# Optimization experiments

Measured on AMD Instinct MI355X. Metric: run time of the kernel, lower is better.

## Reference

```python
import jax, jax.numpy as jnp
import numpy as np

ORDER = 2
TEMP = 1.0
NEG = -9e15


def setup_inputs() -> dict:
    key = jax.random.key(0)
    ks = jax.random.split(key, 12)
    B, D, N, L = 8, 64, 1024, 12
    C_OUT, NH, S = 64, 2, 2
    NOUT = (NH + 1) * ORDER * S + 1  # 13
    sc = 0.05
    x = jax.random.normal(ks[0], (B, D, N, L), jnp.float32)
    A = jax.random.uniform(ks[1], (S, N, N), jnp.float32)
    support = jnp.where(A > 0.9, A, 0.0)
    nv1 = jax.random.normal(ks[2], (N, D), jnp.float32)
    nv2 = jax.random.normal(ks[3], (D, N), jnp.float32)
    key_w = jax.random.normal(ks[4], (NH, 2 * C_OUT, D, L), jnp.float32) * sc
    key_b = jax.random.normal(ks[5], (NH, 2 * C_OUT), jnp.float32) * sc
    query_w = jax.random.normal(ks[6], (NH, 2 * C_OUT, D, L), jnp.float32) * sc
    query_b = jax.random.normal(ks[7], (NH, 2 * C_OUT), jnp.float32) * sc
    attn_w = jax.random.normal(ks[8], (NOUT, D * NOUT), jnp.float32) * sc
    attn_b = jax.random.normal(ks[9], (NOUT,), jnp.float32) * sc
    final_w = jax.random.normal(ks[10], (C_OUT, D), jnp.float32) * sc
    final_b = jax.random.normal(ks[11], (C_OUT,), jnp.float32) * sc
    return {"x": x, "support": support, "nv1": nv1, "nv2": nv2,
            "key_w": key_w, "key_b": key_b, "query_w": query_w, "query_b": query_b,
            "attn_w": attn_w, "attn_b": attn_b, "final_w": final_w, "final_b": final_b}


def reference(x, support, nv1, nv2, key_w, key_b, query_w, query_b,
              attn_w, attn_b, final_w, final_b):
    B, D, N, L = x.shape
    n_head = key_w.shape[0]
    # spatial PE broadcast: nv1 [N,D] -> [1,D,N,1], nv2 [D,N] -> [1,D,N,1]
    nv1_b = nv1.T[None, :, :, None]
    nv2_b = nv2[None, :, :, None]
    out = [x]
    for s in range(support.shape[0]):
        a = support[s]  # [N,N]
        for ih in range(n_head + 1):
            if ih == 0:
                x1 = x
                for _ in range(ORDER):
                    # x2[b,d,w,l] = sum_v x1[b,d,v,l] * a[v,w]
                    x1 = jnp.einsum('bdvl,vw->bdwl', x1, a)
                    out.append(x1)
            else:
                ki = x + nv1_b
                qi = x + nv2_b
                # Conv2d(c_in, 2*c_out, (1,L)) -> [B, 2*c_out, N]
                keys = jnp.einsum('bdnl,edl->ben', ki, key_w[ih - 1]) + key_b[ih - 1][None, :, None]
                query = jnp.einsum('bdnl,edl->ben', qi, query_w[ih - 1]) + query_b[ih - 1][None, :, None]
                e = jax.nn.relu(jnp.einsum('ben,bem->bnm', keys, query))  # [B,N,N]
                att = jnp.where(a[None] > 0, e, NEG) / TEMP
                att = jax.nn.softmax(att, axis=1)  # normalize over source nodes v
                x1 = x
                for _ in range(ORDER):
                    x1 = jnp.einsum('bdvl,bvw->bdwl', x1, att)
                    out.append(x1)
    H = len(out)  # nout
    # per-branch gating attention (is_attention=True)
    feats = jnp.stack([o.mean(axis=(2, 3)) for o in out], axis=1)  # [B,H,D]
    logits = feats.reshape(B, H * D) @ attn_w.T + attn_b  # [B,H]
    gate = jax.nn.softmax(logits / TEMP, axis=1)
    # SUM head aggregation of gated branches
    h = out[0] * gate[:, 0, None, None, None]
    for i in range(1, H):
        h = h + out[i] * gate[:, i, None, None, None]
    # final 1x1 conv
    h = jnp.einsum('bdnl,od->bonl', h, final_w) + final_b[None, :, None, None]
    return h
```

## Files before the change

### kernel.cpp

```cpp
#include <hip/hip_runtime.h>
#include <hip/hip_bf16.h>

#define BB 8
#define DD 64
#define NNODE 1024
#define LLL 12
#define EE 128
#define NEGV -9.0e15f

typedef _Float16 f16;
typedef _Float16 f16x4 __attribute__((ext_vector_type(4)));
typedef _Float16 f16x8 __attribute__((ext_vector_type(8)));
typedef float f32x4 __attribute__((ext_vector_type(4)));


__device__ __forceinline__ void stage_tile(const char* g, int ld, char* lds, int t) {
    int wid = t >> 6, lane = t & 63;
#pragma unroll
    for (int it = 0; it < 4; it++) {
        int cbase = it * 256 + wid * 64;
        int c = cbase + lane;
        int row = c >> 3, p = c & 7;
        int gch = p ^ (row & 7);
        const char* src = g + (size_t)row * ld + gch * 16;
        char* dst = lds + (size_t)cbase * 16;
        __builtin_amdgcn_global_load_lds(
            (const __attribute__((address_space(1))) unsigned int*)src,
            (__attribute__((address_space(3))) unsigned int*)dst, 16, 0, 0);
    }
}

__device__ __forceinline__ void mma_tile(const char* As, const char* Bs, int t,
                                         f32x4 acc[4][4]) {
    int lane = t & 63, wid = t >> 6;
    int wr = (wid >> 1) * 64, wc = (wid & 1) * 64;
    int lrow = lane & 15, lk = lane >> 4;
#pragma unroll
    for (int kk = 0; kk < 2; kk++) {
        f16x8 af[4], bf[4];
#pragma unroll
        for (int m = 0; m < 4; m++) {
            int row = wr + m * 16 + lrow;
            int p = (kk * 4 + lk) ^ (row & 7);
            af[m] = *(const f16x8*)(As + row * 128 + p * 16);
        }
#pragma unroll
        for (int n = 0; n < 4; n++) {
            int row = wc + n * 16 + lrow;
            int p = (kk * 4 + lk) ^ (row & 7);
            bf[n] = *(const f16x8*)(Bs + row * 128 + p * 16);
        }
#pragma unroll
        for (int m = 0; m < 4; m++)
#pragma unroll
            for (int n = 0; n < 4; n++)
                acc[m][n] = __builtin_amdgcn_mfma_f32_16x16x32_f16(
                    af[m], bf[n], acc[m][n], 0, 0, 0);
    }
}

__device__ __forceinline__ void zero_acc(f32x4 acc[4][4]) {
#pragma unroll
    for (int m = 0; m < 4; m++)
#pragma unroll
        for (int n = 0; n < 4; n++)
#pragma unroll
            for (int q = 0; q < 4; q++) acc[m][n][q] = 0.f;
}

__device__ __forceinline__ const f16* pair_B(const f16* aT, const f16* attT,
                                             int j, int b) {
    if (j == 0) return aT;
    if (j == 3) return aT + 1048576;
    int idx = (j < 3) ? (j - 1) : (j - 2);
    return attT + (size_t)idx * 8388608 + (size_t)b * 1048576;
}


__global__ __launch_bounds__(256) void k_xtfused(const float* __restrict__ x,
                                                 f16* __restrict__ XT,
                                                 f16* __restrict__ xT2,
                                                 float* __restrict__ xl) {
    __shared__ f16 Ls[64][210];
    int nt = blockIdx.x, d0 = blockIdx.y * 16, b = blockIdx.z;
    int n0 = nt * 64, t = threadIdx.x;
    for (int f = t; f < 3072; f += 256) {
        int dd = f / 192, rem = f - dd * 192, j = rem / 3, q = rem - j * 3;
        float4 v = *reinterpret_cast<const float4*>(
            x + (((size_t)(b * 64 + d0 + dd) * 1024) + n0 + j) * 12 + q * 4);
        f16* dst = &Ls[j][dd * 12 + q * 4];
        dst[0] = (f16)v.x; dst[1] = (f16)v.y; dst[2] = (f16)v.z; dst[3] = (f16)v.w;
    }
    __syncthreads();
    for (int c = t; c < 12288; c += 256) {
        int row = c >> 6, j = c & 63;
        int dd = row / 12, l = row - dd * 12;
        XT[((size_t)(b * 768) + (size_t)(d0 + dd) * 12 + l) * 1024 + n0 + j] =
            Ls[j][row];
    }
    for (int c = t; c < 1536; c += 256) {
        int j = c / 24, p = c - j * 24;
        *reinterpret_cast<f16x8*>(
            xT2 + ((size_t)(b * 1024) + n0 + j) * 768 + d0 * 12 + p * 8) =
            *reinterpret_cast<const f16x8*>(&Ls[j][p * 8]);
    }
    for (int c = t; c < 1024; c += 256) {
        int dd = c >> 6, j = c & 63;
        float s = 0.f;
#pragma unroll
        for (int l = 0; l < 12; l++) s += (float)Ls[j][dd * 12 + l];
        xl[((size_t)(b * 64 + d0 + dd)) * 1024 + n0 + j] = s;
    }
}

__global__ void k_wcvt(const float* __restrict__ kw, const float* __restrict__ qw,
                       float* __restrict__ kwl, f16* __restrict__ kwb) {
    int i = blockIdx.x * 256 + threadIdx.x;
    int d = i & 63, e = (i >> 6) & 127, var = i >> 13;
    const float* src = (var < 2 ? kw + (size_t)var * 98304
                                : qw + (size_t)(var - 2) * 98304) +
                       ((size_t)e * 64 + d) * 12;
    f16* dst = kwb + ((size_t)var * 128 + e) * 768 + d * 12;
    float ssum = 0.f;
#pragma unroll
    for (int l = 0; l < 12; l++) {
        float v = src[l];
        ssum += v;
        dst[l] = (f16)v;
    }
    kwl[i] = ssum;
}

__global__ void k_tkq(const float* __restrict__ kwl, const float* __restrict__ nv1,
                      const float* __restrict__ nv2, const float* __restrict__ kb,
                      const float* __restrict__ qb, float* __restrict__ tkq) {
    int i = blockIdx.x * 256 + threadIdx.x;
    int e = i & 127, n = (i >> 7) & 1023, var = i >> 17;
    float ssum = (var < 2) ? kb[var * 128 + e] : qb[(var - 2) * 128 + e];
    const float* wl = kwl + ((size_t)var * 128 + e) * 64;
    if (var < 2) {
        const float* nvp = nv1 + (size_t)n * 64;
#pragma unroll 8
        for (int d = 0; d < 64; d++) ssum += wl[d] * nvp[d];
    } else {
#pragma unroll 8
        for (int d = 0; d < 64; d++) ssum += wl[d] * nv2[(size_t)d * 1024 + n];
    }
    tkq[i] = ssum;
}

__global__ void k_acvt(const float* __restrict__ sup, f16* __restrict__ aT) {
    __shared__ float Ls[64][65];
    int s = blockIdx.z, v0 = blockIdx.y * 64, w0 = blockIdx.x * 64, t = threadIdx.x;
    int j = t & 63, i0 = t >> 6;
    for (int i = i0; i < 64; i += 4)
        Ls[i][j] = sup[((size_t)s * 1024 + v0 + i) * 1024 + w0 + j];
    __syncthreads();
    for (int i = i0; i < 64; i += 4)
        aT[((size_t)s * 1024 + w0 + i) * 1024 + v0 + j] = (f16)Ls[j][i];
}


__global__ __launch_bounds__(256) void k_kqgemm(const f16* __restrict__ xT2,
                                                const f16* __restrict__ kwb,
                                                const float* __restrict__ tkq,
                                                f16* __restrict__ keysT) {
    __shared__ char As[16384], Bs[16384];
    int z = blockIdx.z, var = z >> 3, b = z & 7;
    int nt = blockIdx.x, t = threadIdx.x;
    const char* Ag = (const char*)(xT2 + ((size_t)b * 1024 + nt * 128) * 768);
    const char* Bg = (const char*)(kwb + (size_t)var * 128 * 768);
    f32x4 acc[4][4];
    zero_acc(acc);
    for (int kt = 0; kt < 12; kt++) {
        stage_tile(Ag + kt * 128, 1536, As, t);
        stage_tile(Bg + kt * 128, 1536, Bs, t);
        __syncthreads();
        mma_tile(As, Bs, t, acc);
        __syncthreads();
    }
    int lane = t & 63, wid = t >> 6;
    int wr = (wid >> 1) * 64, wc = (wid & 1) * 64;
    int cn = lane & 15, rq = (lane >> 4) * 4;
#pragma unroll
    for (int m = 0; m < 4; m++)
#pragma unroll
        for (int q = 0; q < 4; q++) {
            int n_g = nt * 128 + wr + m * 16 + rq + q;
#pragma unroll
            for (int nn = 0; nn < 4; nn++) {
                int e = wc + nn * 16 + cn;
                float v = acc[m][nn][q] + tkq[((size_t)var * 1024 + n_g) * 128 + e];
                keysT[(((size_t)var * 8 + b) * 1024 + n_g) * 128 + e] = (f16)v;
            }
        }
}

__global__ __launch_bounds__(256) void k_scoregemm2(const f16* __restrict__ keysT,
                                                    f16* __restrict__ scTall) {
    __shared__ char As[16384], Bs[16384];
    int z = blockIdx.z, h = z >> 3, b = z & 7;
    int wt = blockIdx.y, vt = blockIdx.x, t = threadIdx.x;
    const char* Ag = (const char*)(keysT + (((size_t)(2 + h) * 8 + b) * 1024 + wt * 128) * 128);
    const char* Bg = (const char*)(keysT + (((size_t)h * 8 + b) * 1024 + vt * 128) * 128);
    f32x4 acc[4][4];
    zero_acc(acc);
    for (int kt = 0; kt < 2; kt++) {
        stage_tile(Ag + kt * 128, 256, As, t);
        stage_tile(Bg + kt * 128, 256, Bs, t);
        __syncthreads();
        mma_tile(As, Bs, t, acc);
        __syncthreads();
    }
    int lane = t & 63, wid = t >> 6;
    int wr = (wid >> 1) * 64, wc = (wid & 1) * 64;
    int cn = lane & 15, rq = (lane >> 4) * 4;
#pragma unroll
    for (int m = 0; m < 4; m++)
#pragma unroll
        for (int q = 0; q < 4; q++) {
            int w = wt * 128 + wr + m * 16 + rq + q;
#pragma unroll
            for (int nn = 0; nn < 4; nn++) {
                int v = vt * 128 + wc + nn * 16 + cn;
                scTall[((size_t)z * 1024 + w) * 1024 + v] = (f16)fmaxf(acc[m][nn][q], 0.f);
            }
        }
}

__global__ __launch_bounds__(256) void k_prop1m(const f16* __restrict__ ZT,
                                                const f16* __restrict__ aT,
                                                const f16* __restrict__ attT,
                                                f16* __restrict__ P1all) {
    __shared__ char As[16384], Bs[16384];
    int bid = blockIdx.x;
    int swz = (bid & 7) * 288 + (bid >> 3);
    int wt = swz & 7, rt = (swz >> 3) % 6, z = swz / 48;
    int j = z >> 3, b = z & 7;
    int t = threadIdx.x;
    const char* Ag = (const char*)(ZT + ((size_t)b * 768 + rt * 128) * 1024);
    const char* Bg = (const char*)(pair_B(aT, attT, j, b) + (size_t)wt * 128 * 1024);
    f32x4 acc[4][4];
    zero_acc(acc);
    for (int kt = 0; kt < 16; kt++) {
        stage_tile(Ag + kt * 128, 2048, As, t);
        stage_tile(Bg + kt * 128, 2048, Bs, t);
        __syncthreads();
        mma_tile(As, Bs, t, acc);
        __syncthreads();
    }
    f16* P1 = P1all + (size_t)j * 6291456;
    int lane = t & 63, wid = t >> 6;
    int wr = (wid >> 1) * 64, wc = (wid & 1) * 64;
    int cn = lane & 15, rq = (lane >> 4) * 4;
#pragma unroll
    for (int m = 0; m < 4; m++)
#pragma unroll
        for (int q = 0; q < 4; q++) {
            int r = rt * 128 + wr + m * 16 + rq + q;
            size_t pbase = ((size_t)b * 768 + r) * 1024;
#pragma unroll
            for (int nn = 0; nn < 4; nn++) {
                int w = wt * 128 + wc + nn * 16 + cn;
                P1[pbase + w] = (f16)acc[m][nn][q];
            }
        }
}

__global__ __launch_bounds__(256) void k_prop2m(const f16* __restrict__ P1all,
                                                const f16* __restrict__ aT,
                                                const f16* __restrict__ attT,
                                                f16* __restrict__ P2all) {
    __shared__ char As[16384], Bs[16384];
    int bid = blockIdx.x;
    int swz = (bid & 7) * 288 + (bid >> 3);
    int wt = swz & 7, rt = (swz >> 3) % 6, z = swz / 48;
    int j = z >> 3, b = z & 7;
    int t = threadIdx.x;
    const char* Ag = (const char*)(P1all + (size_t)j * 6291456 +
                                   ((size_t)b * 768 + rt * 128) * 1024);
    const char* Bg = (const char*)(pair_B(aT, attT, j, b) + (size_t)wt * 128 * 1024);
    f32x4 acc[4][4];
    zero_acc(acc);
    for (int kt = 0; kt < 16; kt++) {
        stage_tile(Ag + kt * 128, 2048, As, t);
        stage_tile(Bg + kt * 128, 2048, Bs, t);
        __syncthreads();
        mma_tile(As, Bs, t, acc);
        __syncthreads();
    }
    f16* P2 = P2all + (size_t)j * 6291456;
    int lane = t & 63, wid = t >> 6;
    int wr = (wid >> 1) * 64, wc = (wid & 1) * 64;
    int cn = lane & 15, rq = (lane >> 4) * 4;
#pragma unroll
    for (int m = 0; m < 4; m++)
#pragma unroll
        for (int q = 0; q < 4; q++) {
            int r = rt * 128 + wr + m * 16 + rq + q;
            size_t pbase = ((size_t)b * 768 + r) * 1024;
#pragma unroll
            for (int nn = 0; nn < 4; nn++) {
                int w = wt * 128 + wc + nn * 16 + cn;
                P2[pbase + w] = (f16)acc[m][nn][q];
            }
        }
}


__global__ void k_softmax3(const f16* __restrict__ scTall, const f16* __restrict__ aT,
                           f16* __restrict__ attT) {
    int gw = blockIdx.x * 4 + (threadIdx.x >> 6);
    int w = gw & 1023, hb = gw >> 10;
    int h = hb >> 3, b = hb & 7;
    int lane = threadIdx.x & 63;
    const f16* sp = scTall + (size_t)gw * 1024;
    float e[16];
#pragma unroll
    for (int k = 0; k < 16; k++) e[k] = (float)sp[k * 64 + lane];
#pragma unroll
    for (int s = 0; s < 2; s++) {
        const f16* ap = aT + ((size_t)s * 1024 + w) * 1024;
        float xx[16];
        float m = NEGV;
#pragma unroll
        for (int k = 0; k < 16; k++) {
            int v = k * 64 + lane;
            xx[k] = ((float)ap[v] > 0.f) ? e[k] : NEGV;
            m = fmaxf(m, xx[k]);
        }
#pragma unroll
        for (int off = 1; off < 64; off <<= 1) m = fmaxf(m, __shfl_xor(m, off));
        float ssum = 0.f;
#pragma unroll
        for (int k = 0; k < 16; k++) {
            xx[k] = __expf(xx[k] - m);
            ssum += xx[k];
        }
#pragma unroll
        for (int off = 1; off < 64; off <<= 1) ssum += __shfl_xor(ssum, off);
        float inv = 1.f / ssum;
        f16* op = attT + (size_t)(s * 2 + h) * 8388608 +
                  ((size_t)b * 1024 + w) * 1024;
#pragma unroll
        for (int k = 0; k < 16; k++) op[k * 64 + lane] = (f16)(xx[k] * inv);
    }
}

template <int ORDER>
__global__ __launch_bounds__(256) void k_colsum1(
    const f16* __restrict__ aT, const f16* __restrict__ attT,
    const float* __restrict__ ra, const float* __restrict__ ratt,
    float* __restrict__ partial) {
    int u = blockIdx.y, rc = blockIdx.x;
    int t = threadIdx.x;
    int lane7 = t & 127, rh = t >> 7;
    int v0 = lane7 * 8;
    const f16* M = (u < 2) ? aT + (size_t)u * 1048576
                           : attT + (size_t)(u - 2) * 1048576;
    const float* rin = nullptr;
    if (ORDER) rin = (u < 2) ? ra + (size_t)u * 2048 : ratt + (size_t)(u - 2) * 2048;
    float acc[8] = {};
    int row0 = rc * 64 + rh * 32;
#pragma unroll 4
    for (int i = 0; i < 32; i++) {
        int row = row0 + i;
        f16x8 mv = *reinterpret_cast<const f16x8*>(M + (size_t)row * 1024 + v0);
        float sc = ORDER ? rin[row] : 1.f;
#pragma unroll
        for (int j = 0; j < 8; j++) acc[j] += (float)mv[j] * sc;
    }
    float* pp = partial + ((size_t)u * 32 + rc * 2 + rh) * 1024 + v0;
#pragma unroll
    for (int j = 0; j < 8; j++) pp[j] = acc[j];
}

template <int ORDER>
__global__ void k_colsum2(const float* __restrict__ partial, float* __restrict__ ra,
                          float* __restrict__ ratt) {
    int u = blockIdx.x, t = threadIdx.x;
    for (int v = t; v < 1024; v += 256) {
        float s = 0.f;
#pragma unroll
        for (int k = 0; k < 32; k++) s += partial[((size_t)u * 32 + k) * 1024 + v];
        float* out = (u < 2) ? ra + (size_t)u * 2048 : ratt + (size_t)(u - 2) * 2048;
        out[ORDER * 1024 + v] = s;
    }
}

__global__ void k_feat13(const float* __restrict__ xl, const float* __restrict__ ra,
                         const float* __restrict__ ratt, float* __restrict__ feats) {
    int bd = blockIdx.x;
    int b = bd >> 6, d = bd & 63;
    const float* xp = xl + (size_t)bd * 1024;
    int t = threadIdx.x;
    float s[13];
#pragma unroll
    for (int i = 0; i < 13; i++) s[i] = 0.f;
    for (int v = t; v < 1024; v += 256) {
        float xv = xp[v];
        s[0] += xv;
#pragma unroll
        for (int ss = 0; ss < 2; ss++) {
            s[1 + ss * 6 + 0] += xv * ra[ss * 2048 + v];
            s[1 + ss * 6 + 1] += xv * ra[ss * 2048 + 1024 + v];
#pragma unroll
            for (int hh = 0; hh < 2; hh++) {
                const float* rb = ratt + (((size_t)(ss * 2 + hh) * 8 + b)) * 2048;
                s[1 + ss * 6 + 2 + hh * 2] += xv * rb[v];
                s[1 + ss * 6 + 3 + hh * 2] += xv * rb[1024 + v];
            }
        }
    }
    int wid = t >> 6, lane = t & 63;
#pragma unroll
    for (int i = 0; i < 13; i++)
#pragma unroll
        for (int off = 1; off < 64; off <<= 1) s[i] += __shfl_xor(s[i], off);
    __shared__ float red[13][4];
    if (lane == 0)
#pragma unroll
        for (int i = 0; i < 13; i++) red[i][wid] = s[i];
    __syncthreads();
    if (t < 13) {
        float tot = red[t][0] + red[t][1] + red[t][2] + red[t][3];
        feats[(size_t)b * 832 + t * 64 + d] = tot * (1.f / (1024.f * 12.f));
    }
}

__global__ void k_gate(const float* __restrict__ feats, const float* __restrict__ aw,
                       const float* __restrict__ ab, float* __restrict__ gate) {
    int b = blockIdx.x, t = threadIdx.x;
    __shared__ float lg[13];
    if (t < 13) {
        float s = ab[t];
        const float* f = feats + (size_t)b * 832;
        const float* w = aw + (size_t)t * 832;
        for (int k = 0; k < 832; k++) s += f[k] * w[k];
        lg[t] = s;
    }
    __syncthreads();
    if (t == 0) {
        float m = lg[0];
        for (int j = 1; j < 13; j++) m = fmaxf(m, lg[j]);
        float ss = 0.f;
        for (int j = 0; j < 13; j++) ss += __expf(lg[j] - m);
        float inv = 1.f / ss;
        for (int j = 0; j < 13; j++) gate[b * 13 + j] = __expf(lg[j] - m) * inv;
    }
}

__global__ __launch_bounds__(256) void k_zt2(f16* __restrict__ XT,
                                             const float* __restrict__ fw) {
    __shared__ f16 xs[64][136];
    __shared__ float fws[64][64];
    int nt = blockIdx.x, l = blockIdx.y, b = blockIdx.z;
    int t = threadIdx.x;
    f16* base = XT + (size_t)b * 786432 + (size_t)l * 1024 + nt * 128;
#pragma unroll
    for (int it = 0; it < 4; it++) {
        int idx = it * 256 + t;
        int row = idx >> 4, c = idx & 15;
        *reinterpret_cast<f16x8*>(&xs[row][c * 8]) =
            *reinterpret_cast<const f16x8*>(base + (size_t)row * 12288 + c * 8);
    }
    for (int i = t; i < 4096; i += 256) ((float*)fws)[i] = fw[i];
    __syncthreads();
    int nl = t & 31, og = t >> 5;
    float acc[8][4];
#pragma unroll
    for (int oo = 0; oo < 8; oo++)
#pragma unroll
        for (int j = 0; j < 4; j++) acc[oo][j] = 0.f;
#pragma unroll 4
    for (int d = 0; d < 64; d++) {
        f16x4 xv = *reinterpret_cast<const f16x4*>(&xs[d][nl * 4]);
        float x0 = (float)xv[0], x1 = (float)xv[1], x2 = (float)xv[2], x3 = (float)xv[3];
#pragma unroll
        for (int oo = 0; oo < 8; oo++) {
            float w = fws[og * 8 + oo][d];
            acc[oo][0] += w * x0; acc[oo][1] += w * x1;
            acc[oo][2] += w * x2; acc[oo][3] += w * x3;
        }
    }
#pragma unroll
    for (int oo = 0; oo < 8; oo++) {
        int o = og * 8 + oo;
        f16x4 ov;
        ov[0] = (f16)acc[oo][0]; ov[1] = (f16)acc[oo][1];
        ov[2] = (f16)acc[oo][2]; ov[3] = (f16)acc[oo][3];
        *reinterpret_cast<f16x4*>(base + (size_t)o * 12288 + nl * 4) = ov;
    }
}

__global__ void k_out(const f16* __restrict__ ZT, const f16* __restrict__ P1all,
                      const f16* __restrict__ P2all, const float* __restrict__ gate,
                      const float* __restrict__ fb, float* __restrict__ out) {
    int idx = blockIdx.x * 256 + threadIdx.x;
    int n = idx & 1023, o = (idx >> 10) & 63, b = idx >> 16;
    const float* g = gate + b * 13;
    size_t rowbase = ((size_t)b * 768 + o * 12) * 1024 + n;
    float v[12];
    float g0 = g[0], fbv = fb[o];
#pragma unroll
    for (int l = 0; l < 12; l++)
        v[l] = fbv + g0 * (float)ZT[rowbase + (size_t)l * 1024];
#pragma unroll
    for (int j = 0; j < 6; j++) {
        float g1 = g[1 + 2 * j], g2 = g[2 + 2 * j];
        const f16* p1 = P1all + (size_t)j * 6291456 + rowbase;
        const f16* p2 = P2all + (size_t)j * 6291456 + rowbase;
#pragma unroll
        for (int l = 0; l < 12; l++)
            v[l] += g1 * (float)p1[(size_t)l * 1024] + g2 * (float)p2[(size_t)l * 1024];
    }
    float4* dst = reinterpret_cast<float4*>(out + (((size_t)b * 64 + o) * 1024 + n) * 12);
    float4 o0 = {v[0], v[1], v[2], v[3]};
    float4 o1 = {v[4], v[5], v[6], v[7]};
    float4 o2 = {v[8], v[9], v[10], v[11]};
    dst[0] = o0; dst[1] = o1; dst[2] = o2;
}


extern "C" void kernel_launch(void* const* d_in, const int* in_sizes, int n_in,
                              void* d_out, int out_size, void* d_ws, size_t ws_size,
                              hipStream_t stream) {
    const float* x   = (const float*)d_in[0];
    const float* sup = (const float*)d_in[1];
    const float* nv1 = (const float*)d_in[2];
    const float* nv2 = (const float*)d_in[3];
    const float* kw  = (const float*)d_in[4];
    const float* kb  = (const float*)d_in[5];
    const float* qw  = (const float*)d_in[6];
    const float* qb  = (const float*)d_in[7];
    const float* aw  = (const float*)d_in[8];
    const float* ab  = (const float*)d_in[9];
    const float* fw  = (const float*)d_in[10];
    const float* fb  = (const float*)d_in[11];
    float* hout = (float*)d_out;

    float* wsf = (float*)d_ws;
    size_t o = 0;
    f16*   XT     = (f16*)(wsf + o);  o += 3145728;
    float* attReg = wsf + o;          o += 16777216;
    f16*   attT   = (f16*)attReg;
    f16*   xT2    = (f16*)attReg;
    f16*   aT     = (f16*)(wsf + o);  o += 1048576;
    float* gate   = wsf + o;          o += 128;
    size_t rc = o;
    size_t oA = rc;
    f16*   scTall = (f16*)(wsf + oA);  oA += 8388608;
    f16*   keysT  = (f16*)(wsf + oA);  oA += 2097152;
    f16*   kwb    = (f16*)(wsf + oA);  oA += 196608;
    float* kwl    = wsf + oA;          oA += 32768;
    float* tkq    = wsf + oA;          oA += 524288;
    float* xl     = wsf + oA;          oA += 524288;
    float* ra     = wsf + oA;          oA += 4096;
    float* ratt   = wsf + oA;          oA += 65536;
    float* feats  = wsf + oA;          oA += 6656;
    float* partial= wsf + oA;          oA += 1114112;
    size_t oB = rc;
    f16*   P1all  = (f16*)(wsf + oB); oB += 18874368;
    f16*   P2all  = (f16*)(wsf + oB); oB += 18874368;
    size_t need = ((oA > oB) ? oA : oB) * 4;
    if (ws_size < need) return;

    f16* ZT = XT;

    k_xtfused<<<dim3(16, 4, 8), 256, 0, stream>>>(x, XT, xT2, xl);
    k_wcvt<<<128, 256, 0, stream>>>(kw, qw, kwl, kwb);
    k_tkq<<<2048, 256, 0, stream>>>(kwl, nv1, nv2, kb, qb, tkq);
    k_acvt<<<dim3(16, 16, 2), 256, 0, stream>>>(sup, aT);

    k_kqgemm<<<dim3(8, 1, 32), 256, 0, stream>>>(xT2, kwb, tkq, keysT);

    k_scoregemm2<<<dim3(8, 8, 16), 256, 0, stream>>>(keysT, scTall);
    k_softmax3<<<4096, 256, 0, stream>>>(scTall, aT, attT);

    k_colsum1<0><<<dim3(16, 34), 256, 0, stream>>>(aT, attT, ra, ratt, partial);
    k_colsum2<0><<<34, 256, 0, stream>>>(partial, ra, ratt);
    k_colsum1<1><<<dim3(16, 34), 256, 0, stream>>>(aT, attT, ra, ratt, partial);
    k_colsum2<1><<<34, 256, 0, stream>>>(partial, ra, ratt);
    k_feat13<<<512, 256, 0, stream>>>(xl, ra, ratt, feats);
    k_gate<<<8, 64, 0, stream>>>(feats, aw, ab, gate);

    k_zt2<<<dim3(8, 12, 8), 256, 0, stream>>>(XT, fw);

    k_prop1m<<<2304, 256, 0, stream>>>(ZT, aT, attT, P1all);
    k_prop2m<<<2304, 256, 0, stream>>>(P1all, aT, attT, P2all);
    k_out<<<2048, 256, 0, stream>>>(ZT, P1all, P2all, gate, fb, hout);
}
```

Before: 369.8 us.

## Vectorize memory accesses across kernels and halve kqgemm row tile

Several kernels get wider memory accesses. The XT transpose writes f16x4 instead of scalars, and softmax loads and stores contiguous f16x8 chunks per lane instead of strided scalars. colsum partials are stored as float4, and k_out processes two nodes per thread with f16x2 loads. Separately, k_kqgemm drops to 64-row tiles with twice as many blocks, to raise occupancy and parallelism on the small GEMM. This cuts load and store instruction count and makes accesses better coalesced, at the cost of higher per-thread register use in k_out.

```diff
diff --git a/kernel.cpp b/kernel.cpp
--- a/kernel.cpp
+++ b/kernel.cpp
@@ -9,6 +9,7 @@
 #define NEGV -9.0e15f
 
 typedef _Float16 f16;
+typedef _Float16 f16x2 __attribute__((ext_vector_type(2)));
 typedef _Float16 f16x4 __attribute__((ext_vector_type(4)));
 typedef _Float16 f16x8 __attribute__((ext_vector_type(8)));
 typedef float f32x4 __attribute__((ext_vector_type(4)));
@@ -92,11 +93,14 @@
         dst[0] = (f16)v.x; dst[1] = (f16)v.y; dst[2] = (f16)v.z; dst[3] = (f16)v.w;
     }
     __syncthreads();
-    for (int c = t; c < 12288; c += 256) {
-        int row = c >> 6, j = c & 63;
+    for (int c = t; c < 3072; c += 256) {
+        int row = c >> 4, j4 = c & 15;
         int dd = row / 12, l = row - dd * 12;
-        XT[((size_t)(b * 768) + (size_t)(d0 + dd) * 12 + l) * 1024 + n0 + j] =
-            Ls[j][row];
+        f16x4 v;
+#pragma unroll
+        for (int q = 0; q < 4; q++) v[q] = Ls[j4 * 4 + q][row];
+        *reinterpret_cast<f16x4*>(
+            &XT[((size_t)(b * 768) + (size_t)(d0 + dd) * 12 + l) * 1024 + n0 + j4 * 4]) = v;
     }
     for (int c = t; c < 1536; c += 256) {
         int j = c / 24, p = c - j * 24;
@@ -165,28 +169,66 @@
                                                 const f16* __restrict__ kwb,
                                                 const float* __restrict__ tkq,
                                                 f16* __restrict__ keysT) {
-    __shared__ char As[16384], Bs[16384];
+    __shared__ char As[8192], Bs[16384];
     int z = blockIdx.z, var = z >> 3, b = z & 7;
     int nt = blockIdx.x, t = threadIdx.x;
-    const char* Ag = (const char*)(xT2 + ((size_t)b * 1024 + nt * 128) * 768);
+    const char* Ag = (const char*)(xT2 + ((size_t)b * 1024 + nt * 64) * 768);
     const char* Bg = (const char*)(kwb + (size_t)var * 128 * 768);
-    f32x4 acc[4][4];
-    zero_acc(acc);
+    f32x4 acc[2][4];
+#pragma unroll
+    for (int m = 0; m < 2; m++)
+#pragma unroll
+        for (int n = 0; n < 4; n++)
+#pragma unroll
+            for (int q = 0; q < 4; q++) acc[m][n][q] = 0.f;
+    int lane = t & 63, wid = t >> 6;
+    int lrow = lane & 15, lk = lane >> 4;
+    int wr = (wid >> 1) * 32, wc = (wid & 1) * 64;
     for (int kt = 0; kt < 12; kt++) {
-        stage_tile(Ag + kt * 128, 1536, As, t);
+#pragma unroll
+        for (int it = 0; it < 2; it++) {
+            int cbase = it * 256 + wid * 64;
+            int c = cbase + lane;
+            int row = c >> 3, p = c & 7;
+            int gch = p ^ (row & 7);
+            const char* src = Ag + kt * 128 + (size_t)row * 1536 + gch * 16;
+            char* dst = As + (size_t)cbase * 16;
+            __builtin_amdgcn_global_load_lds(
+                (const __attribute__((address_space(1))) unsigned int*)src,
+                (__attribute__((address_space(3))) unsigned int*)dst, 16, 0, 0);
+        }
         stage_tile(Bg + kt * 128, 1536, Bs, t);
         __syncthreads();
-        mma_tile(As, Bs, t, acc);
-        __syncthreads();
-    }
-    int lane = t & 63, wid = t >> 6;
-    int wr = (wid >> 1) * 64, wc = (wid & 1) * 64;
+#pragma unroll
+        for (int kk = 0; kk < 2; kk++) {
+            f16x8 af[2], bf[4];
+#pragma unroll
+            for (int m = 0; m < 2; m++) {
+                int row = wr + m * 16 + lrow;
+                int p = (kk * 4 + lk) ^ (row & 7);
+                af[m] = *(const f16x8*)(As + row * 128 + p * 16);
+            }
+#pragma unroll
+            for (int n = 0; n < 4; n++) {
+                int row = wc + n * 16 + lrow;
+                int p = (kk * 4 + lk) ^ (row & 7);
+                bf[n] = *(const f16x8*)(Bs + row * 128 + p * 16);
+            }
+#pragma unroll
+            for (int m = 0; m < 2; m++)
+#pragma unroll
+                for (int n = 0; n < 4; n++)
+                    acc[m][n] = __builtin_amdgcn_mfma_f32_16x16x32_f16(
+                        af[m], bf[n], acc[m][n], 0, 0, 0);
+        }
+        __syncthreads();
+    }
     int cn = lane & 15, rq = (lane >> 4) * 4;
 #pragma unroll
-    for (int m = 0; m < 4; m++)
+    for (int m = 0; m < 2; m++)
 #pragma unroll
         for (int q = 0; q < 4; q++) {
-            int n_g = nt * 128 + wr + m * 16 + rq + q;
+            int n_g = nt * 64 + wr + m * 16 + rq + q;
 #pragma unroll
             for (int nn = 0; nn < 4; nn++) {
                 int e = wc + nn * 16 + cn;
@@ -314,21 +356,23 @@
     int w = gw & 1023, hb = gw >> 10;
     int h = hb >> 3, b = hb & 7;
     int lane = threadIdx.x & 63;
-    const f16* sp = scTall + (size_t)gw * 1024;
-    float e[16];
-#pragma unroll
-    for (int k = 0; k < 16; k++) e[k] = (float)sp[k * 64 + lane];
+    const f16* sp = scTall + (size_t)gw * 1024 + lane * 16;
+    f16x8 e0 = *reinterpret_cast<const f16x8*>(sp);
+    f16x8 e1 = *reinterpret_cast<const f16x8*>(sp + 8);
 #pragma unroll
     for (int s = 0; s < 2; s++) {
-        const f16* ap = aT + ((size_t)s * 1024 + w) * 1024;
+        const f16* ap = aT + ((size_t)s * 1024 + w) * 1024 + lane * 16;
+        f16x8 a0 = *reinterpret_cast<const f16x8*>(ap);
+        f16x8 a1 = *reinterpret_cast<const f16x8*>(ap + 8);
         float xx[16];
         float m = NEGV;
 #pragma unroll
-        for (int k = 0; k < 16; k++) {
-            int v = k * 64 + lane;
-            xx[k] = ((float)ap[v] > 0.f) ? e[k] : NEGV;
-            m = fmaxf(m, xx[k]);
-        }
+        for (int k = 0; k < 8; k++) {
+            xx[k]     = ((float)a0[k] > 0.f) ? (float)e0[k] : NEGV;
+            xx[8 + k] = ((float)a1[k] > 0.f) ? (float)e1[k] : NEGV;
+        }
+#pragma unroll
+        for (int k = 0; k < 16; k++) m = fmaxf(m, xx[k]);
 #pragma unroll
         for (int off = 1; off < 64; off <<= 1) m = fmaxf(m, __shfl_xor(m, off));
         float ssum = 0.f;
@@ -340,10 +384,16 @@
 #pragma unroll
         for (int off = 1; off < 64; off <<= 1) ssum += __shfl_xor(ssum, off);
         float inv = 1.f / ssum;
+        f16x8 o0, o1;
+#pragma unroll
+        for (int k = 0; k < 8; k++) {
+            o0[k] = (f16)(xx[k] * inv);
+            o1[k] = (f16)(xx[8 + k] * inv);
+        }
         f16* op = attT + (size_t)(s * 2 + h) * 8388608 +
-                  ((size_t)b * 1024 + w) * 1024;
-#pragma unroll
-        for (int k = 0; k < 16; k++) op[k * 64 + lane] = (f16)(xx[k] * inv);
+                  ((size_t)b * 1024 + w) * 1024 + lane * 16;
+        *reinterpret_cast<f16x8*>(op) = o0;
+        *reinterpret_cast<f16x8*>(op + 8) = o1;
     }
 }
 
@@ -370,9 +420,11 @@
 #pragma unroll
         for (int j = 0; j < 8; j++) acc[j] += (float)mv[j] * sc;
     }
-    float* pp = partial + ((size_t)u * 32 + rc * 2 + rh) * 1024 + v0;
-#pragma unroll
-    for (int j = 0; j < 8; j++) pp[j] = acc[j];
+    float4* pp = reinterpret_cast<float4*>(
+        partial + ((size_t)u * 32 + rc * 2 + rh) * 1024 + v0);
+    float4 w0 = {acc[0], acc[1], acc[2], acc[3]};
+    float4 w1 = {acc[4], acc[5], acc[6], acc[7]};
+    pp[0] = w0; pp[1] = w1;
 }
 
 template <int ORDER>
@@ -497,28 +549,40 @@
                       const f16* __restrict__ P2all, const float* __restrict__ gate,
                       const float* __restrict__ fb, float* __restrict__ out) {
     int idx = blockIdx.x * 256 + threadIdx.x;
-    int n = idx & 1023, o = (idx >> 10) & 63, b = idx >> 16;
+    int n2 = idx & 511, o = (idx >> 9) & 63, b = idx >> 15;
+    int n = n2 * 2;
     const float* g = gate + b * 13;
     size_t rowbase = ((size_t)b * 768 + o * 12) * 1024 + n;
-    float v[12];
     float g0 = g[0], fbv = fb[o];
-#pragma unroll
-    for (int l = 0; l < 12; l++)
-        v[l] = fbv + g0 * (float)ZT[rowbase + (size_t)l * 1024];
+    float v0[12], v1[12];
+#pragma unroll
+    for (int l = 0; l < 12; l++) {
+        f16x2 z2 = *reinterpret_cast<const f16x2*>(&ZT[rowbase + (size_t)l * 1024]);
+        v0[l] = fbv + g0 * (float)z2[0];
+        v1[l] = fbv + g0 * (float)z2[1];
+    }
 #pragma unroll
     for (int j = 0; j < 6; j++) {
         float g1 = g[1 + 2 * j], g2 = g[2 + 2 * j];
         const f16* p1 = P1all + (size_t)j * 6291456 + rowbase;
         const f16* p2 = P2all + (size_t)j * 6291456 + rowbase;
 #pragma unroll
-        for (int l = 0; l < 12; l++)
-            v[l] += g1 * (float)p1[(size_t)l * 1024] + g2 * (float)p2[(size_t)l * 1024];
-    }
-    float4* dst = reinterpret_cast<float4*>(out + (((size_t)b * 64 + o) * 1024 + n) * 12);
-    float4 o0 = {v[0], v[1], v[2], v[3]};
-    float4 o1 = {v[4], v[5], v[6], v[7]};
-    float4 o2 = {v[8], v[9], v[10], v[11]};
-    dst[0] = o0; dst[1] = o1; dst[2] = o2;
+        for (int l = 0; l < 12; l++) {
+            f16x2 a2 = *reinterpret_cast<const f16x2*>(&p1[(size_t)l * 1024]);
+            f16x2 b2 = *reinterpret_cast<const f16x2*>(&p2[(size_t)l * 1024]);
+            v0[l] += g1 * (float)a2[0] + g2 * (float)b2[0];
+            v1[l] += g1 * (float)a2[1] + g2 * (float)b2[1];
+        }
+    }
+    float4* dst0 = reinterpret_cast<float4*>(out + (((size_t)b * 64 + o) * 1024 + n) * 12);
+    float4 a0 = {v0[0], v0[1], v0[2], v0[3]};
+    float4 a1 = {v0[4], v0[5], v0[6], v0[7]};
+    float4 a2 = {v0[8], v0[9], v0[10], v0[11]};
+    dst0[0] = a0; dst0[1] = a1; dst0[2] = a2;
+    float4 b0 = {v1[0], v1[1], v1[2], v1[3]};
+    float4 b1 = {v1[4], v1[5], v1[6], v1[7]};
+    float4 b2 = {v1[8], v1[9], v1[10], v1[11]};
+    dst0[3] = b0; dst0[4] = b1; dst0[5] = b2;
 }
 
 
@@ -572,7 +636,7 @@
     k_tkq<<<2048, 256, 0, stream>>>(kwl, nv1, nv2, kb, qb, tkq);
     k_acvt<<<dim3(16, 16, 2), 256, 0, stream>>>(sup, aT);
 
-    k_kqgemm<<<dim3(8, 1, 32), 256, 0, stream>>>(xT2, kwb, tkq, keysT);
+    k_kqgemm<<<dim3(16, 1, 32), 256, 0, stream>>>(xT2, kwb, tkq, keysT);
 
     k_scoregemm2<<<dim3(8, 8, 16), 256, 0, stream>>>(keysT, scTall);
     k_softmax3<<<4096, 256, 0, stream>>>(scTall, aT, attT);
@@ -588,5 +652,5 @@
 
     k_prop1m<<<2304, 256, 0, stream>>>(ZT, aT, attT, P1all);
     k_prop2m<<<2304, 256, 0, stream>>>(P1all, aT, attT, P2all);
-    k_out<<<2048, 256, 0, stream>>>(ZT, P1all, P2all, gate, fb, hout);
-}
+    k_out<<<1024, 256, 0, stream>>>(ZT, P1all, P2all, gate, fb, hout);
+}
```

Result: slower. 403.8 us (+9.2%).
